# Kernel optimization log

Measured on AMD Instinct MI355X. Metric: run time of the kernel, lower is better.

Reference implementation:

```python
import jax, jax.numpy as jnp
import numpy as np

N, E, G = 150000, 600000, 5000
NI, EI, GF, H, C = 16, 8, 32, 64, 40


def setup_inputs() -> dict:
    key = jax.random.key(0)
    ks = jax.random.split(key, 20)
    s = lambda fan: 1.0 / np.sqrt(fan)
    return {
        "x": jax.random.normal(ks[0], (N, NI), jnp.float32),
        "edge_index": jax.random.randint(ks[1], (2, E), 0, N),
        "edge_attr": jax.random.normal(ks[2], (E, EI), jnp.float32),
        "batch": jnp.sort(jax.random.randint(ks[3], (N,), 0, G)),
        "pocket_features": jax.random.normal(ks[4], (G, GF), jnp.float32),
        # edge MLP: Linear(EI,H) -> ReLU -> Linear(H, H*NI)
        "W_e1": jax.random.normal(ks[5], (EI, H), jnp.float32) * s(EI),
        "b_e1": jnp.zeros((H,), jnp.float32),
        "W_e2": jax.random.normal(ks[6], (H, H * NI), jnp.float32) * s(H),
        "b_e2": jnp.zeros((H * NI,), jnp.float32),
        # NNConv root weight + bias
        "root": jax.random.normal(ks[7], (NI, H), jnp.float32) * s(NI),
        "conv_bias": jnp.zeros((H,), jnp.float32),
        # GlobalAttention gate Linear(H,1)
        "Wg": jax.random.normal(ks[8], (H, 1), jnp.float32) * s(H),
        "bg": jnp.zeros((1,), jnp.float32),
        # fc1: input is concat [h_node(H), global_ctx(H), pocket(GF)]
        "W_fc1": jax.random.normal(ks[9], (2 * H + GF, H), jnp.float32) * s(2 * H + GF),
        "b_fc1": jnp.zeros((H,), jnp.float32),
        "W_np": jax.random.normal(ks[10], (H, C), jnp.float32) * s(H),
        "b_np": jnp.zeros((C,), jnp.float32),
        "W_sp": jax.random.normal(ks[11], (H, 1), jnp.float32) * s(H),
        "b_sp": jnp.zeros((1,), jnp.float32),
    }


def reference(x, edge_index, edge_attr, batch, pocket_features,
              W_e1, b_e1, W_e2, b_e2, root, conv_bias, Wg, bg,
              W_fc1, b_fc1, W_np, b_np, W_sp, b_sp):
    n, ni = x.shape
    h = root.shape[1]
    g = pocket_features.shape[0]
    src, dst = edge_index[0], edge_index[1]

    # NNConv: edge MLP -> per-edge weight matrix [E, NI, H]
    eh = jax.nn.relu(edge_attr @ W_e1 + b_e1)
    We = (eh @ W_e2 + b_e2).reshape(-1, ni, h)
    msg = jnp.einsum('ei,eih->eh', x[src], We)          # per-edge matmul
    agg = jax.ops.segment_sum(msg, dst, num_segments=n)
    cnt = jax.ops.segment_sum(jnp.ones(msg.shape[0], x.dtype), dst, num_segments=n)
    agg = agg / jnp.maximum(cnt, 1.0)[:, None]          # aggr='mean'
    h_node = jax.nn.relu(agg + x @ root + conv_bias)    # [N, H]

    # GlobalAttention pooling: scatter-softmax over nodes per graph
    gate = (h_node @ Wg + bg).squeeze(-1)               # [N]
    m = jax.ops.segment_max(gate, batch, num_segments=g)
    e = jnp.exp(gate - m[batch])
    denom = jax.ops.segment_sum(e, batch, num_segments=g)
    attn = e / denom[batch]
    gctx = jax.ops.segment_sum(attn[:, None] * h_node, batch, num_segments=g)
    gc = gctx[batch]                                    # broadcast back [N, H]

    feat = jnp.concatenate([h_node, gc, pocket_features[batch]], axis=1)
    f = jax.nn.relu(feat @ W_fc1 + b_fc1)
    node_pred = jax.nn.log_softmax(f @ W_np + b_np, axis=-1)
    stop = jax.nn.sigmoid((gc @ W_sp + b_sp).squeeze(-1))
    return node_pred, stop
```

## Files before the change

kernel.cpp:

```cpp
#include <hip/hip_runtime.h>
#include <hip/hip_bf16.h>
#include <math.h>

#define NN 150000
#define EE 600000
#define GG 5000
#define NI 16
#define EI 8
#define GFD 32
#define HH 64
#define CC 40

#define W2SZ (68 * 1024)
#define EHS 72
#define FPAD 68
#define NBLK ((NN + 1023) / 1024)

typedef __attribute__((ext_vector_type(8))) short short8v;
typedef __attribute__((ext_vector_type(8))) unsigned short ushort8v;
typedef __attribute__((ext_vector_type(16))) float f32x16;
typedef __attribute__((ext_vector_type(2))) float f32x2;

__device__ __forceinline__ unsigned short f2bf(float f) {
    __hip_bfloat16 h = __float2bfloat16(f);
    return __builtin_bit_cast(unsigned short, h);
}
__device__ __forceinline__ float bf2f(unsigned short u) {
    return __uint_as_float(((unsigned)u) << 16);
}
__device__ __forceinline__ unsigned cvtpk(float lo, float hi) {
    unsigned r;
    asm("v_cvt_pk_bf16_f32 %0, %1, %2" : "=v"(r) : "v"(lo), "v"(hi));
    return r;
}
__device__ __forceinline__ f32x2 pkmul(f32x2 a, f32x2 b) {
    f32x2 p;
    asm("v_pk_mul_f32 %0, %1, %2" : "=v"(p) : "v"(a), "v"(b));
    return p;
}
__device__ __forceinline__ short8v zfrag(float eh, const f32x2 (&xs2)[4]) {
    f32x2 ehp; ehp[0] = eh; ehp[1] = eh;
    union { short8v v; unsigned u[4]; } A;
    #pragma unroll
    for (int q = 0; q < 4; ++q) {
        f32x2 p = pkmul(ehp, xs2[q]);
        A.u[q] = cvtpk(p[0], p[1]);
    }
    return A.v;
}
__device__ __forceinline__ short8v xfrag(const f32x2 (&xs2)[4]) {
    union { short8v v; unsigned u[4]; } A;
    #pragma unroll
    for (int q = 0; q < 4; ++q)
        A.u[q] = cvtpk(xs2[q][0], xs2[q][1]);
    return A.v;
}

__global__ void k0_prep(const float* __restrict__ W_e2, const float* __restrict__ b_e2,
                        const float* __restrict__ W_fc1, const float* __restrict__ W_np,
                        const float* __restrict__ W_e1,
                        unsigned short* __restrict__ W2c,
                        unsigned short* __restrict__ W1aT,
                        unsigned short* __restrict__ W_npT,
                        unsigned short* __restrict__ W1e,
                        int* __restrict__ cursor)
{
    int idx = blockIdx.x * 256 + threadIdx.x;
    if (idx < W2SZ) {
        int c = idx >> 10, rem = idx & 1023;
        int r = rem >> 4, kk = rem & 15;
        float v = 0.f;
        if (c < 64)       v = W_e2[c * 1024 + kk * 64 + r];
        else if (c == 64) v = b_e2[kk * 64 + r];
        W2c[idx] = f2bf(v);
    } else if (idx < W2SZ + 4096) {
        int i = idx - W2SZ;
        int h = i >> 6, k = i & 63;
        W1aT[i] = f2bf(W_fc1[k * 64 + h]);
    } else if (idx < W2SZ + 8192) {
        int i = idx - W2SZ - 4096;
        int c = i >> 6, h = i & 63;
        W_npT[i] = f2bf(c < CC ? W_np[h * CC + c] : 0.f);
    } else if (idx < W2SZ + 8704) {
        int i = idx - W2SZ - 8192;
        int col = i >> 3, q = i & 7;
        W1e[i] = f2bf(W_e1[q * 64 + col]);
    } else if (idx < W2SZ + 8704 + NN) {
        cursor[idx - W2SZ - 8704] = 0;
    }
}

__global__ void kE_local(const int* __restrict__ ei, int* __restrict__ cursor,
                         int* __restrict__ rank)
{
    int e = blockIdx.x * 256 + threadIdx.x;
    if (e < EE) rank[e] = atomicAdd(&cursor[ei[EE + e]], 1);
}

__global__ void kB_scan1(const int* __restrict__ cnt, int* __restrict__ base,
                         int* __restrict__ bsum)
{
    __shared__ int sS[256];
    int b = blockIdx.x, t = threadIdx.x;
    int i0 = b * 1024 + t * 4;
    int v0 = (i0 + 0 < NN) ? cnt[i0 + 0] : 0;
    int v1 = (i0 + 1 < NN) ? cnt[i0 + 1] : 0;
    int v2 = (i0 + 2 < NN) ? cnt[i0 + 2] : 0;
    int v3 = (i0 + 3 < NN) ? cnt[i0 + 3] : 0;
    int tot = v0 + v1 + v2 + v3;
    sS[t] = tot;
    __syncthreads();
    int acc = tot;
    for (int off = 1; off < 256; off <<= 1) {
        int xv = (t >= off) ? sS[t - off] : 0;
        __syncthreads();
        acc += xv;
        sS[t] = acc;
        __syncthreads();
    }
    int run = acc - tot;
    if (i0 + 0 < NN) base[i0 + 0] = run; run += v0;
    if (i0 + 1 < NN) base[i0 + 1] = run; run += v1;
    if (i0 + 2 < NN) base[i0 + 2] = run; run += v2;
    if (i0 + 3 < NN) base[i0 + 3] = run;
    if (t == 255) bsum[b] = acc;
}

__global__ void kC_scan2(int* __restrict__ bsum)
{
    __shared__ int sS[256];
    int t = threadIdx.x;
    int v = (t < NBLK) ? bsum[t] : 0;
    sS[t] = v;
    __syncthreads();
    int acc = v;
    for (int off = 1; off < 256; off <<= 1) {
        int xv = (t >= off) ? sS[t - off] : 0;
        __syncthreads();
        acc += xv;
        sS[t] = acc;
        __syncthreads();
    }
    if (t < NBLK) bsum[t] = acc - v;
}

template<bool TWOPHASE>
__global__ __launch_bounds__(256, 5) void k1_mfma(
    const float* __restrict__ x, const int* __restrict__ ei,
    const float* __restrict__ ea,
    const unsigned short* __restrict__ W1e, const float* __restrict__ b_e1,
    const unsigned short* __restrict__ W2c,
    const int* __restrict__ rank, const int* __restrict__ base,
    const int* __restrict__ bsum,
    unsigned* __restrict__ msg16, float* __restrict__ agg)
{
    __shared__ unsigned short sEHT2[128][EHS];
    __shared__ int sIdx[128];

    const int t = threadIdx.x;
    const long long eb = (long long)blockIdx.x * 128;

    const int lane = t & 63;
    const int w = t >> 6;
    const int mr = lane & 31;
    const int half = lane >> 5;
    const int mb2 = w * 32;

    if (t < 128) {
        long long ge = eb + t;
        if (ge < EE) {
            int d = ei[EE + ge];
            sIdx[t] = TWOPHASE ? (base[d] + bsum[d >> 10] + rank[ge]) : d;
        } else {
            sIdx[t] = -1;
        }
    }

    {
        short8v bW0, bW1;
        if (half == 0) {
            bW0 = *(const short8v*)(W1e + (size_t)mr * 8);
            bW1 = *(const short8v*)(W1e + (size_t)(32 + mr) * 8);
        } else {
            #pragma unroll
            for (int q = 0; q < 8; ++q) { bW0[q] = 0; bW1[q] = 0; }
        }
        float bias0 = b_e1[mr];
        float bias1 = b_e1[32 + mr];
        long long ge = eb + mb2 + mr;
        short8v a;
        if (half == 0 && ge < EE) {
            const float4* eap = (const float4*)(ea + ge * EI);
            float4 u0 = eap[0], u1 = eap[1];
            union { short8v v; unsigned u[4]; } A;
            A.u[0] = cvtpk(u0.x, u0.y); A.u[1] = cvtpk(u0.z, u0.w);
            A.u[2] = cvtpk(u1.x, u1.y); A.u[3] = cvtpk(u1.z, u1.w);
            a = A.v;
        } else {
            #pragma unroll
            for (int q = 0; q < 8; ++q) a[q] = 0;
        }
        #pragma unroll
        for (int n = 0; n < 2; ++n) {
            f32x16 c_;
            #pragma unroll
            for (int r = 0; r < 16; ++r) c_[r] = 0.f;
            c_ = __builtin_amdgcn_mfma_f32_32x32x16_bf16(a, n ? bW1 : bW0, c_, 0, 0, 0);
            int kcol = n * 32 + mr;
            float bias = n ? bias1 : bias0;
            #pragma unroll
            for (int r = 0; r < 16; ++r) {
                int row = (r & 3) + 8 * (r >> 2) + 4 * half;
                sEHT2[mb2 + row][kcol] = f2bf(fmaxf(c_[r] + bias, 0.f));
            }
        }
    }

    f32x2 xs[4];
    {
        long long ge = eb + mb2 + mr;
        if (ge < EE) {
            int s0 = ei[ge];
            const float4* xp = (const float4*)(x + (size_t)s0 * NI + half * 8);
            float4 u0 = xp[0], u1 = xp[1];
            xs[0][0]=u0.x; xs[0][1]=u0.y; xs[1][0]=u0.z; xs[1][1]=u0.w;
            xs[2][0]=u1.x; xs[2][1]=u1.y; xs[3][0]=u1.z; xs[3][1]=u1.w;
        } else {
            #pragma unroll
            for (int q = 0; q < 4; ++q) { xs[q][0] = 0.f; xs[q][1] = 0.f; }
        }
    }
    __syncthreads();

    f32x16 acc0, acc1;
    #pragma unroll
    for (int r = 0; r < 16; ++r) { acc0[r] = 0.f; acc1[r] = 0.f; }

    const unsigned short* Bq0 = W2c + mr * 16 + half * 8;
    const unsigned short* Bq1 = Bq0 + 512;

    short8v bA0 = *(const short8v*)(Bq0);
    short8v bA1 = *(const short8v*)(Bq1);
    short8v bB0 = *(const short8v*)(Bq0 + 1024);
    short8v bB1 = *(const short8v*)(Bq1 + 1024);

    const unsigned short* ehp = &sEHT2[mb2 + mr][0];
    ushort8v ehCur = *(const ushort8v*)(ehp);

    #pragma unroll 1
    for (int cb = 0; cb < 64; cb += 8) {
        ushort8v ehNext = *(const ushort8v*)(ehp + cb + 8);
        #pragma unroll
        for (int j = 0; j < 8; j += 2) {
            int c = cb + j;
            {
                short8v n0 = *(const short8v*)(Bq0 + (c + 2) * 1024);
                short8v n1 = *(const short8v*)(Bq1 + (c + 2) * 1024);
                short8v a = zfrag(bf2f(ehCur[j]), xs);
                __builtin_amdgcn_s_setprio(1);
                acc0 = __builtin_amdgcn_mfma_f32_32x32x16_bf16(a, bA0, acc0, 0, 0, 0);
                acc1 = __builtin_amdgcn_mfma_f32_32x32x16_bf16(a, bA1, acc1, 0, 0, 0);
                __builtin_amdgcn_s_setprio(0);
                bA0 = n0; bA1 = n1;
            }
            {
                short8v n0 = *(const short8v*)(Bq0 + (c + 3) * 1024);
                short8v n1 = *(const short8v*)(Bq1 + (c + 3) * 1024);
                short8v a = zfrag(bf2f(ehCur[j + 1]), xs);
                __builtin_amdgcn_s_setprio(1);
                acc0 = __builtin_amdgcn_mfma_f32_32x32x16_bf16(a, bB0, acc0, 0, 0, 0);
                acc1 = __builtin_amdgcn_mfma_f32_32x32x16_bf16(a, bB1, acc1, 0, 0, 0);
                __builtin_amdgcn_s_setprio(0);
                bB0 = n0; bB1 = n1;
            }
        }
        ehCur = ehNext;
    }
    {
        short8v a = xfrag(xs);
        __builtin_amdgcn_s_setprio(1);
        acc0 = __builtin_amdgcn_mfma_f32_32x32x16_bf16(a, bA0, acc0, 0, 0, 0);
        acc1 = __builtin_amdgcn_mfma_f32_32x32x16_bf16(a, bA1, acc1, 0, 0, 0);
        __builtin_amdgcn_s_setprio(0);
    }

    #pragma unroll
    for (int r = 0; r < 16; ++r) {
        int row = (r & 3) + 8 * (r >> 2) + 4 * half;
        int i0 = sIdx[mb2 + row];
        if (TWOPHASE) {
            if (i0 >= 0) msg16[(size_t)i0 * 32 + mr] = cvtpk(acc0[r], acc1[r]);
        } else {
            if (i0 >= 0) {
                atomicAdd(&agg[(size_t)i0 * 64 + mr],      acc0[r]);
                atomicAdd(&agg[(size_t)i0 * 64 + 32 + mr], acc1[r]);
            }
        }
    }
}

__global__ __launch_bounds__(256) void k2_red(
    const unsigned* __restrict__ msg16, const int* __restrict__ base,
    const int* __restrict__ bsum,
    const float* __restrict__ x, const float* __restrict__ root,
    const float* __restrict__ conv_bias,
    unsigned short* __restrict__ hn16,
    const float* __restrict__ Wg, const float* __restrict__ bg,
    float* __restrict__ gate)
{
    __shared__ float sroot[16][64];
    int t = threadIdx.x;
    #pragma unroll
    for (int q = 0; q < 4; ++q) {
        int i = q * 256 + t;
        sroot[i >> 6][i & 63] = root[i];
    }
    __syncthreads();

    int n = blockIdx.x * 4 + (t >> 6);
    int l = t & 63;
    int mr = l & 31, so = l >> 5;
    int s = base[n] + bsum[n >> 10];
    int e = (n == NN - 1) ? EE : base[n + 1] + bsum[(n + 1) >> 10];

    float alo = 0.f, ahi = 0.f;
    int sl = s + so;
    for (; sl + 2 < e; sl += 4) {
        unsigned u0 = msg16[(size_t)sl * 32 + mr];
        unsigned u1 = msg16[(size_t)(sl + 2) * 32 + mr];
        alo += __uint_as_float(u0 << 16) + __uint_as_float(u1 << 16);
        ahi += __uint_as_float(u0 & 0xFFFF0000u) + __uint_as_float(u1 & 0xFFFF0000u);
    }
    if (sl < e) {
        unsigned u = msg16[(size_t)sl * 32 + mr];
        alo += __uint_as_float(u << 16);
        ahi += __uint_as_float(u & 0xFFFF0000u);
    }
    alo += __shfl_xor(alo, 32);
    ahi += __shfl_xor(ahi, 32);
    float acc = (l < 32) ? alo : ahi;

    float inv = 1.0f / fmaxf((float)(e - s), 1.0f);
    float v = acc * inv + conv_bias[l];
    float xv = (l < 16) ? x[(size_t)n * NI + l] : 0.f;
    #pragma unroll
    for (int i = 0; i < 16; ++i)
        v = fmaf(__shfl(xv, i), sroot[i][l], v);
    v = fmaxf(v, 0.f);
    hn16[(size_t)n * 64 + l] = f2bf(v);

    float gv = v * Wg[l];
    #pragma unroll
    for (int off = 32; off; off >>= 1) gv += __shfl_xor(gv, off);
    if (l == 0) gate[n] = gv + bg[0];
}

__global__ __launch_bounds__(256) void k2_node(
    const float* __restrict__ agg, const int* __restrict__ base,
    const int* __restrict__ bsum,
    const float* __restrict__ x, const float* __restrict__ root,
    const float* __restrict__ conv_bias,
    unsigned short* __restrict__ hn16,
    const float* __restrict__ Wg, const float* __restrict__ bg,
    float* __restrict__ gate)
{
    int t = threadIdx.x;
    int n = blockIdx.x * 4 + (t >> 6);
    int h = t & 63;
    int s = base[n] + bsum[n >> 10];
    int e = (n == NN - 1) ? EE : base[n + 1] + bsum[(n + 1) >> 10];
    float inv = 1.0f / fmaxf((float)(e - s), 1.0f);
    float v = agg[(size_t)n * 64 + h] * inv + conv_bias[h];
    const float* xp = x + (size_t)n * NI;
    #pragma unroll
    for (int i = 0; i < NI; ++i) v += xp[i] * root[i * 64 + h];
    v = fmaxf(v, 0.f);
    hn16[(size_t)n * 64 + h] = f2bf(v);
    float gv = v * Wg[h];
    #pragma unroll
    for (int off = 32; off; off >>= 1) gv += __shfl_xor(gv, off);
    if (h == 0) gate[n] = gv + bg[0];
}

__device__ __forceinline__ int lbound(const int* __restrict__ b, int v) {
    int lo = 0, hi = NN;
    while (lo < hi) { int mid = (lo + hi) >> 1; if (b[mid] < v) lo = mid + 1; else hi = mid; }
    return lo;
}

__global__ __launch_bounds__(64) void k3_pool(
    const float* __restrict__ gate, const int* __restrict__ batch,
    const unsigned short* __restrict__ hn16, const float* __restrict__ pocket,
    const float* __restrict__ W_fc1, const float* __restrict__ b_fc1,
    const float* __restrict__ W_sp, const float* __restrict__ b_sp,
    float* __restrict__ pg, float* __restrict__ sg)
{
    int g = blockIdx.x;
    int lane = threadIdx.x;
    int s = lbound(batch, g);
    int e = lbound(batch, g + 1);

    float gcv = 0.f;
    if (e > s) {
        float m = -INFINITY;
        for (int n = s + lane; n < e; n += 64) m = fmaxf(m, gate[n]);
        #pragma unroll
        for (int off = 32; off; off >>= 1) m = fmaxf(m, __shfl_xor(m, off));
        float acc = 0.f, den = 0.f;
        int n = s;
        for (; n + 2 <= e; n += 2) {
            float e0 = expf(gate[n] - m);
            float e1 = expf(gate[n + 1] - m);
            float h0 = bf2f(hn16[(size_t)n * 64 + lane]);
            float h1 = bf2f(hn16[(size_t)(n + 1) * 64 + lane]);
            den += e0 + e1;
            acc = fmaf(e0, h0, acc);
            acc = fmaf(e1, h1, acc);
        }
        if (n < e) {
            float ev = expf(gate[n] - m);
            den += ev;
            acc = fmaf(ev, bf2f(hn16[(size_t)n * 64 + lane]), acc);
        }
        gcv = acc / den;
    }

    float sv = gcv * W_sp[lane];
    #pragma unroll
    for (int off = 32; off; off >>= 1) sv += __shfl_xor(sv, off);
    if (lane == 0) sg[g] = 1.f / (1.f + expf(-(sv + b_sp[0])));

    float pk = (lane < GFD) ? pocket[(size_t)g * GFD + lane] : 0.f;
    float pgv = b_fc1[lane];
    #pragma unroll 8
    for (int kk = 0; kk < 64; ++kk)
        pgv = fmaf(__shfl(gcv, kk), W_fc1[(64 + kk) * 64 + lane], pgv);
    #pragma unroll 8
    for (int kk = 0; kk < 32; ++kk)
        pgv = fmaf(__shfl(pk, kk), W_fc1[(128 + kk) * 64 + lane], pgv);
    pg[(size_t)g * 64 + lane] = pgv;
}

__global__ __launch_bounds__(256, 4) void k4_mfma(
    const unsigned short* __restrict__ hn16, const int* __restrict__ batch,
    const float* __restrict__ pg, const float* __restrict__ sg,
    const unsigned short* __restrict__ W1aT, const unsigned short* __restrict__ W_npT,
    const float* __restrict__ b_np,
    float* __restrict__ out_np, float* __restrict__ out_stop)
{
    __shared__ __align__(16) float sF[4][32][FPAD];
    __shared__ int sB[128];

    const int t = threadIdx.x;
    const int wv = t >> 6, lane = t & 63;
    const int mr = lane & 31, half = lane >> 5;
    const int nb = blockIdx.x * 128;

    if (t < 128) {
        int n = nb + t;
        sB[t] = (n < NN) ? batch[n] : 0;
    }

    const int node = nb + wv * 32 + mr;

    f32x16 acc0, acc1;
    #pragma unroll
    for (int r = 0; r < 16; ++r) { acc0[r] = 0.f; acc1[r] = 0.f; }

    #pragma unroll
    for (int c = 0; c < 4; ++c) {
        short8v a;
        if (node < NN) {
            a = *(const short8v*)(hn16 + (size_t)node * 64 + c * 16 + half * 8);
        } else {
            #pragma unroll
            for (int q = 0; q < 8; ++q) a[q] = 0;
        }
        short8v b0 = *(const short8v*)(W1aT + (size_t)mr * 64        + c * 16 + half * 8);
        short8v b1 = *(const short8v*)(W1aT + (size_t)(mr + 32) * 64 + c * 16 + half * 8);
        acc0 = __builtin_amdgcn_mfma_f32_32x32x16_bf16(a, b0, acc0, 0, 0, 0);
        acc1 = __builtin_amdgcn_mfma_f32_32x32x16_bf16(a, b1, acc1, 0, 0, 0);
    }
    __syncthreads();

    #pragma unroll
    for (int r = 0; r < 16; ++r) {
        int row = (r & 3) + 8 * (r >> 2) + 4 * half;
        int g = sB[wv * 32 + row];
        float p0 = pg[(size_t)g * 64 + mr];
        float p1 = pg[(size_t)g * 64 + 32 + mr];
        sF[wv][row][mr]      = fmaxf(acc0[r] + p0, 0.f);
        sF[wv][row][32 + mr] = fmaxf(acc1[r] + p1, 0.f);
    }

    f32x16 acc2, acc3;
    #pragma unroll
    for (int r = 0; r < 16; ++r) { acc2[r] = 0.f; acc3[r] = 0.f; }

    #pragma unroll
    for (int c = 0; c < 4; ++c) {
        const float* fp = &sF[wv][mr][c * 16 + half * 8];
        float4 u0 = *(const float4*)(fp);
        float4 u1 = *(const float4*)(fp + 4);
        union { short8v v; unsigned u[4]; } A;
        A.u[0] = cvtpk(u0.x, u0.y); A.u[1] = cvtpk(u0.z, u0.w);
        A.u[2] = cvtpk(u1.x, u1.y); A.u[3] = cvtpk(u1.z, u1.w);
        short8v a = A.v;
        short8v b0 = *(const short8v*)(W_npT + (size_t)mr * 64        + c * 16 + half * 8);
        short8v b1 = *(const short8v*)(W_npT + (size_t)(mr + 32) * 64 + c * 16 + half * 8);
        acc2 = __builtin_amdgcn_mfma_f32_32x32x16_bf16(a, b0, acc2, 0, 0, 0);
        acc3 = __builtin_amdgcn_mfma_f32_32x32x16_bf16(a, b1, acc3, 0, 0, 0);
    }

    float bn1 = b_np[mr];
    float bn2 = (mr < 8) ? b_np[32 + mr] : 0.f;

    #pragma unroll
    for (int r = 0; r < 16; ++r) {
        int row = (r & 3) + 8 * (r >> 2) + 4 * half;
        int n = nb + wv * 32 + row;
        float v1 = acc2[r] + bn1;
        float v2 = acc3[r] + bn2;
        float m = (mr < 8) ? fmaxf(v1, v2) : v1;
        #pragma unroll
        for (int off = 16; off; off >>= 1) m = fmaxf(m, __shfl_xor(m, off));
        float s = expf(v1 - m) + ((mr < 8) ? expf(v2 - m) : 0.f);
        #pragma unroll
        for (int off = 16; off; off >>= 1) s += __shfl_xor(s, off);
        float ls = m + logf(s);
        if (n < NN) {
            out_np[(size_t)n * CC + mr] = v1 - ls;
            if (mr < 8) out_np[(size_t)n * CC + 32 + mr] = v2 - ls;
            if (mr == 0) out_stop[n] = sg[sB[wv * 32 + row]];
        }
    }
}

extern "C" void kernel_launch(void* const* d_in, const int* in_sizes, int n_in,
                              void* d_out, int out_size, void* d_ws, size_t ws_size,
                              hipStream_t stream)
{
    (void)in_sizes; (void)n_in; (void)out_size;
    const float* x        = (const float*)d_in[0];
    const int*   ei       = (const int*)d_in[1];
    const float* ea       = (const float*)d_in[2];
    const int*   batch    = (const int*)d_in[3];
    const float* pocket   = (const float*)d_in[4];
    const float* W_e1     = (const float*)d_in[5];
    const float* b_e1     = (const float*)d_in[6];
    const float* W_e2     = (const float*)d_in[7];
    const float* b_e2     = (const float*)d_in[8];
    const float* root     = (const float*)d_in[9];
    const float* conv_b   = (const float*)d_in[10];
    const float* Wg       = (const float*)d_in[11];
    const float* bg       = (const float*)d_in[12];
    const float* W_fc1    = (const float*)d_in[13];
    const float* b_fc1    = (const float*)d_in[14];
    const float* W_np     = (const float*)d_in[15];
    const float* b_np     = (const float*)d_in[16];
    const float* W_sp     = (const float*)d_in[17];
    const float* b_sp     = (const float*)d_in[18];

    char* wsb = (char*)d_ws;
    float* agg    = (float*)wsb;
    int*   base   = (int*)(agg + (size_t)NN * 64);
    int*   bsum   = base + NN + 4;
    int*   cursor = bsum + 256;
    int*   rank   = cursor + NN;
    float* gate   = (float*)(rank + EE);
    float* pg     = gate + NN;
    float* sg     = pg + (size_t)GG * 64;
    unsigned short* hn16  = (unsigned short*)(sg + GG);
    unsigned short* W2c   = hn16 + (size_t)NN * 64;
    unsigned short* W1aT  = W2c + W2SZ;
    unsigned short* W_npT = W1aT + 4096;
    unsigned short* W1e   = W_npT + 4096;
    size_t head = (size_t)((char*)(W1e + 512) - wsb);
    size_t msg_off = (head + 255) & ~(size_t)255;
    unsigned* msg16 = (unsigned*)(wsb + msg_off);
    size_t need = msg_off + (size_t)EE * 32 * sizeof(unsigned);
    const bool twophase = (ws_size >= need);

    k0_prep<<<(W2SZ + 8704 + NN + 255) / 256, 256, 0, stream>>>(
        W_e2, b_e2, W_fc1, W_np, W_e1, W2c, W1aT, W_npT, W1e, cursor);

    kE_local<<<(EE + 255) / 256, 256, 0, stream>>>(ei, cursor, rank);
    kB_scan1<<<NBLK, 256, 0, stream>>>(cursor, base, bsum);
    kC_scan2<<<1, 256, 0, stream>>>(bsum);

    if (twophase) {
        k1_mfma<true><<<(EE + 127) / 128, 256, 0, stream>>>(
            x, ei, ea, W1e, b_e1, W2c, rank, base, bsum, msg16, agg);
        k2_red<<<NN / 4, 256, 0, stream>>>(msg16, base, bsum, x, root, conv_b,
                                           hn16, Wg, bg, gate);
    } else {
        hipMemsetAsync(agg, 0, (size_t)NN * 64 * sizeof(float), stream);
        k1_mfma<false><<<(EE + 127) / 128, 256, 0, stream>>>(
            x, ei, ea, W1e, b_e1, W2c, rank, base, bsum, msg16, agg);
        k2_node<<<NN / 4, 256, 0, stream>>>(agg, base, bsum, x, root, conv_b,
                                            hn16, Wg, bg, gate);
    }

    k3_pool<<<GG, 64, 0, stream>>>(gate, batch, hn16, pocket, W_fc1, b_fc1, W_sp, b_sp, pg, sg);

    float* out_np   = (float*)d_out;
    float* out_stop = out_np + (size_t)NN * CC;
    k4_mfma<<<(NN + 127) / 128, 256, 0, stream>>>(hn16, batch, pg, sg, W1aT, W_npT, b_np,
                                                  out_np, out_stop);
}
```

Before: 255.1 us.

## Split per-edge MFMA work so each wave reuses one weight fragment across two edge tiles

The edge-message MFMA kernel now assigns each wave one 32-column half of the output and two 32-edge tiles, rather than 32 edges and all 64 columns. Each B fragment of the expanded edge weight is loaded once and used for two MFMAs, which halves the per-wave weight loads from global/cache. The cost is loading two source-node feature sets and building two A fragments per step, plus storing messages as separate bf16 halves (2-byte stores instead of packed 4-byte). The reduce kernel gets an extra shuffle to restore channel order.

```diff
diff --git a/kernel.cpp b/kernel.cpp
--- a/kernel.cpp
+++ b/kernel.cpp
@@ -152,7 +152,7 @@
     const unsigned short* __restrict__ W2c,
     const int* __restrict__ rank, const int* __restrict__ base,
     const int* __restrict__ bsum,
-    unsigned* __restrict__ msg16, float* __restrict__ agg)
+    unsigned short* __restrict__ msgb, float* __restrict__ agg)
 {
     __shared__ unsigned short sEHT2[128][EHS];
     __shared__ int sIdx[128];
@@ -164,7 +164,9 @@
     const int w = t >> 6;
     const int mr = lane & 31;
     const int half = lane >> 5;
-    const int mb2 = w * 32;
+    const int egrp = w >> 1;
+    const int nhalf = w & 1;
+    const int mlp_eb = w * 32;
 
     if (t < 128) {
         long long ge = eb + t;
@@ -187,7 +189,7 @@
         }
         float bias0 = b_e1[mr];
         float bias1 = b_e1[32 + mr];
-        long long ge = eb + mb2 + mr;
+        long long ge = eb + mlp_eb + mr;
         short8v a;
         if (half == 0 && ge < EE) {
             const float4* eap = (const float4*)(ea + ge * EI);
@@ -211,23 +213,34 @@
             #pragma unroll
             for (int r = 0; r < 16; ++r) {
                 int row = (r & 3) + 8 * (r >> 2) + 4 * half;
-                sEHT2[mb2 + row][kcol] = f2bf(fmaxf(c_[r] + bias, 0.f));
+                sEHT2[mlp_eb + row][kcol] = f2bf(fmaxf(c_[r] + bias, 0.f));
             }
         }
     }
 
-    f32x2 xs[4];
+    f32x2 xs0[4], xs1[4];
     {
-        long long ge = eb + mb2 + mr;
-        if (ge < EE) {
-            int s0 = ei[ge];
+        long long g0 = eb + egrp * 64 + mr;
+        long long g1 = g0 + 32;
+        if (g0 < EE) {
+            int s0 = ei[g0];
             const float4* xp = (const float4*)(x + (size_t)s0 * NI + half * 8);
             float4 u0 = xp[0], u1 = xp[1];
-            xs[0][0]=u0.x; xs[0][1]=u0.y; xs[1][0]=u0.z; xs[1][1]=u0.w;
-            xs[2][0]=u1.x; xs[2][1]=u1.y; xs[3][0]=u1.z; xs[3][1]=u1.w;
+            xs0[0][0]=u0.x; xs0[0][1]=u0.y; xs0[1][0]=u0.z; xs0[1][1]=u0.w;
+            xs0[2][0]=u1.x; xs0[2][1]=u1.y; xs0[3][0]=u1.z; xs0[3][1]=u1.w;
         } else {
             #pragma unroll
-            for (int q = 0; q < 4; ++q) { xs[q][0] = 0.f; xs[q][1] = 0.f; }
+            for (int q = 0; q < 4; ++q) { xs0[q][0] = 0.f; xs0[q][1] = 0.f; }
+        }
+        if (g1 < EE) {
+            int s1 = ei[g1];
+            const float4* xp = (const float4*)(x + (size_t)s1 * NI + half * 8);
+            float4 u0 = xp[0], u1 = xp[1];
+            xs1[0][0]=u0.x; xs1[0][1]=u0.y; xs1[1][0]=u0.z; xs1[1][1]=u0.w;
+            xs1[2][0]=u1.x; xs1[2][1]=u1.y; xs1[3][0]=u1.z; xs1[3][1]=u1.w;
+        } else {
+            #pragma unroll
+            for (int q = 0; q < 4; ++q) { xs1[q][0] = 0.f; xs1[q][1] = 0.f; }
         }
     }
     __syncthreads();
@@ -236,71 +249,69 @@
     #pragma unroll
     for (int r = 0; r < 16; ++r) { acc0[r] = 0.f; acc1[r] = 0.f; }
 
-    const unsigned short* Bq0 = W2c + mr * 16 + half * 8;
-    const unsigned short* Bq1 = Bq0 + 512;
-
-    short8v bA0 = *(const short8v*)(Bq0);
-    short8v bA1 = *(const short8v*)(Bq1);
-    short8v bB0 = *(const short8v*)(Bq0 + 1024);
-    short8v bB1 = *(const short8v*)(Bq1 + 1024);
-
-    const unsigned short* ehp = &sEHT2[mb2 + mr][0];
-    ushort8v ehCur = *(const ushort8v*)(ehp);
+    const unsigned short* Bq = W2c + nhalf * 512 + mr * 16 + half * 8;
+
+    short8v bA = *(const short8v*)(Bq);
+    short8v bB = *(const short8v*)(Bq + 1024);
+
+    const unsigned short* ehp0 = &sEHT2[egrp * 64 + mr][0];
+    const unsigned short* ehp1 = ehp0 + 32 * EHS;
 
     #pragma unroll 1
     for (int cb = 0; cb < 64; cb += 8) {
-        ushort8v ehNext = *(const ushort8v*)(ehp + cb + 8);
+        ushort8v eh0 = *(const ushort8v*)(ehp0 + cb);
+        ushort8v eh1 = *(const ushort8v*)(ehp1 + cb);
         #pragma unroll
         for (int j = 0; j < 8; j += 2) {
             int c = cb + j;
             {
-                short8v n0 = *(const short8v*)(Bq0 + (c + 2) * 1024);
-                short8v n1 = *(const short8v*)(Bq1 + (c + 2) * 1024);
-                short8v a = zfrag(bf2f(ehCur[j]), xs);
+                short8v nx = *(const short8v*)(Bq + (c + 2) * 1024);
+                short8v a0 = zfrag(bf2f(eh0[j]), xs0);
+                short8v a1 = zfrag(bf2f(eh1[j]), xs1);
                 __builtin_amdgcn_s_setprio(1);
-                acc0 = __builtin_amdgcn_mfma_f32_32x32x16_bf16(a, bA0, acc0, 0, 0, 0);
-                acc1 = __builtin_amdgcn_mfma_f32_32x32x16_bf16(a, bA1, acc1, 0, 0, 0);
+                acc0 = __builtin_amdgcn_mfma_f32_32x32x16_bf16(a0, bA, acc0, 0, 0, 0);
+                acc1 = __builtin_amdgcn_mfma_f32_32x32x16_bf16(a1, bA, acc1, 0, 0, 0);
                 __builtin_amdgcn_s_setprio(0);
-                bA0 = n0; bA1 = n1;
+                bA = nx;
             }
             {
-                short8v n0 = *(const short8v*)(Bq0 + (c + 3) * 1024);
-                short8v n1 = *(const short8v*)(Bq1 + (c + 3) * 1024);
-                short8v a = zfrag(bf2f(ehCur[j + 1]), xs);
+                short8v nx = *(const short8v*)(Bq + (c + 3) * 1024);
+                short8v a0 = zfrag(bf2f(eh0[j + 1]), xs0);
+                short8v a1 = zfrag(bf2f(eh1[j + 1]), xs1);
                 __builtin_amdgcn_s_setprio(1);
-                acc0 = __builtin_amdgcn_mfma_f32_32x32x16_bf16(a, bB0, acc0, 0, 0, 0);
-                acc1 = __builtin_amdgcn_mfma_f32_32x32x16_bf16(a, bB1, acc1, 0, 0, 0);
+                acc0 = __builtin_amdgcn_mfma_f32_32x32x16_bf16(a0, bB, acc0, 0, 0, 0);
+                acc1 = __builtin_amdgcn_mfma_f32_32x32x16_bf16(a1, bB, acc1, 0, 0, 0);
                 __builtin_amdgcn_s_setprio(0);
-                bB0 = n0; bB1 = n1;
+                bB = nx;
             }
         }
-        ehCur = ehNext;
     }
     {
-        short8v a = xfrag(xs);
+        short8v a0 = xfrag(xs0);
+        short8v a1 = xfrag(xs1);
         __builtin_amdgcn_s_setprio(1);
-        acc0 = __builtin_amdgcn_mfma_f32_32x32x16_bf16(a, bA0, acc0, 0, 0, 0);
-        acc1 = __builtin_amdgcn_mfma_f32_32x32x16_bf16(a, bA1, acc1, 0, 0, 0);
+        acc0 = __builtin_amdgcn_mfma_f32_32x32x16_bf16(a0, bA, acc0, 0, 0, 0);
+        acc1 = __builtin_amdgcn_mfma_f32_32x32x16_bf16(a1, bA, acc1, 0, 0, 0);
         __builtin_amdgcn_s_setprio(0);
     }
 
     #pragma unroll
     for (int r = 0; r < 16; ++r) {
         int row = (r & 3) + 8 * (r >> 2) + 4 * half;
-        int i0 = sIdx[mb2 + row];
+        int i0 = sIdx[egrp * 64 + row];
+        int i1 = sIdx[egrp * 64 + 32 + row];
         if (TWOPHASE) {
-            if (i0 >= 0) msg16[(size_t)i0 * 32 + mr] = cvtpk(acc0[r], acc1[r]);
+            if (i0 >= 0) msgb[(size_t)i0 * 64 + nhalf * 32 + mr] = f2bf(acc0[r]);
+            if (i1 >= 0) msgb[(size_t)i1 * 64 + nhalf * 32 + mr] = f2bf(acc1[r]);
         } else {
-            if (i0 >= 0) {
-                atomicAdd(&agg[(size_t)i0 * 64 + mr],      acc0[r]);
-                atomicAdd(&agg[(size_t)i0 * 64 + 32 + mr], acc1[r]);
-            }
+            if (i0 >= 0) atomicAdd(&agg[(size_t)i0 * 64 + nhalf * 32 + mr], acc0[r]);
+            if (i1 >= 0) atomicAdd(&agg[(size_t)i1 * 64 + nhalf * 32 + mr], acc1[r]);
         }
     }
 }
 
 __global__ __launch_bounds__(256) void k2_red(
-    const unsigned* __restrict__ msg16, const int* __restrict__ base,
+    const unsigned short* __restrict__ msgb, const int* __restrict__ base,
     const int* __restrict__ bsum,
     const float* __restrict__ x, const float* __restrict__ root,
     const float* __restrict__ conv_bias,
@@ -317,28 +328,31 @@
     }
     __syncthreads();
 
+    const unsigned* msgu = (const unsigned*)msgb;
     int n = blockIdx.x * 4 + (t >> 6);
     int l = t & 63;
-    int mr = l & 31, so = l >> 5;
+    int m = l & 31, so = l >> 5;
     int s = base[n] + bsum[n >> 10];
     int e = (n == NN - 1) ? EE : base[n + 1] + bsum[(n + 1) >> 10];
 
     float alo = 0.f, ahi = 0.f;
     int sl = s + so;
     for (; sl + 2 < e; sl += 4) {
-        unsigned u0 = msg16[(size_t)sl * 32 + mr];
-        unsigned u1 = msg16[(size_t)(sl + 2) * 32 + mr];
+        unsigned u0 = msgu[(size_t)sl * 32 + m];
+        unsigned u1 = msgu[(size_t)(sl + 2) * 32 + m];
         alo += __uint_as_float(u0 << 16) + __uint_as_float(u1 << 16);
         ahi += __uint_as_float(u0 & 0xFFFF0000u) + __uint_as_float(u1 & 0xFFFF0000u);
     }
     if (sl < e) {
-        unsigned u = msg16[(size_t)sl * 32 + mr];
+        unsigned u = msgu[(size_t)sl * 32 + m];
         alo += __uint_as_float(u << 16);
         ahi += __uint_as_float(u & 0xFFFF0000u);
     }
     alo += __shfl_xor(alo, 32);
     ahi += __shfl_xor(ahi, 32);
-    float acc = (l < 32) ? alo : ahi;
+    float alo_s = __shfl(alo, l >> 1);
+    float ahi_s = __shfl(ahi, l >> 1);
+    float acc = (l & 1) ? ahi_s : alo_s;
 
     float inv = 1.0f / fmaxf((float)(e - s), 1.0f);
     float v = acc * inv + conv_bias[l];
@@ -577,8 +591,8 @@
     unsigned short* W1e   = W_npT + 4096;
     size_t head = (size_t)((char*)(W1e + 512) - wsb);
     size_t msg_off = (head + 255) & ~(size_t)255;
-    unsigned* msg16 = (unsigned*)(wsb + msg_off);
-    size_t need = msg_off + (size_t)EE * 32 * sizeof(unsigned);
+    unsigned short* msgb = (unsigned short*)(wsb + msg_off);
+    size_t need = msg_off + (size_t)EE * 64 * sizeof(unsigned short);
     const bool twophase = (ws_size >= need);
 
     k0_prep<<<(W2SZ + 8704 + NN + 255) / 256, 256, 0, stream>>>(
@@ -590,13 +604,13 @@
 
     if (twophase) {
         k1_mfma<true><<<(EE + 127) / 128, 256, 0, stream>>>(
-            x, ei, ea, W1e, b_e1, W2c, rank, base, bsum, msg16, agg);
-        k2_red<<<NN / 4, 256, 0, stream>>>(msg16, base, bsum, x, root, conv_b,
+            x, ei, ea, W1e, b_e1, W2c, rank, base, bsum, msgb, agg);
+        k2_red<<<NN / 4, 256, 0, stream>>>(msgb, base, bsum, x, root, conv_b,
                                            hn16, Wg, bg, gate);
     } else {
         hipMemsetAsync(agg, 0, (size_t)NN * 64 * sizeof(float), stream);
         k1_mfma<false><<<(EE + 127) / 128, 256, 0, stream>>>(
-            x, ei, ea, W1e, b_e1, W2c, rank, base, bsum, msg16, agg);
+            x, ei, ea, W1e, b_e1, W2c, rank, base, bsum, msgb, agg);
         k2_node<<<NN / 4, 256, 0, stream>>>(agg, base, bsum, x, root, conv_b,
                                             hn16, Wg, bg, gate);
     }
```

Result: slower. 262.9 us (+3.0%).
